# Optimization experiments

Measured on AMD Instinct MI355X. Metric: run time of the kernel, lower is better.

## Reference

```python
import jax, jax.numpy as jnp
from jax import lax
import numpy as np

Vw, Vc, TAGS = 50000, 200, 600
WE, CE, CC, H = 128, 48, 64, 256   # word emb, char emb, char cnn out, encoder hidden
B, T, CL, LMAX = 64, 96, 16, 24    # batch, seq, chars-per-word, lemma max len
HD = H // 2                        # per-direction LSTM hidden
BOS = 3


def _conv1d_same(x, w, b):
    # x: [N, Cin, L], w: [Cout, Cin, K] -> [N, Cout, L]
    y = lax.conv_general_dilated(x, w, (1,), 'SAME', dimension_numbers=('NCH', 'OIH', 'NCH'))
    return y + b[None, :, None]


def _lstm(x, wih, whh, b, reverse):
    # x: [B, T, D]; torch-gate-order LSTM (i, f, g, o); returns [B, T, HD]
    n = x.shape[0]
    def step(carry, xt):
        h, c = carry
        g = xt @ wih.T + h @ whh.T + b
        i, f, gg, o = jnp.split(g, 4, axis=-1)
        c = jax.nn.sigmoid(f) * c + jax.nn.sigmoid(i) * jnp.tanh(gg)
        h = jax.nn.sigmoid(o) * jnp.tanh(c)
        return (h, c), h
    init = (jnp.zeros((n, HD), x.dtype), jnp.zeros((n, HD), x.dtype))
    _, hs = lax.scan(step, init, jnp.swapaxes(x, 0, 1), reverse=reverse)
    return jnp.swapaxes(hs, 0, 1)


def setup_inputs() -> dict:
    key = jax.random.key(0)
    ks = jax.random.split(key, 26)
    g = lambda k, shape: jax.random.normal(k, shape, jnp.float32) * 0.05
    d = {}
    d['word_ids'] = jax.random.randint(ks[0], (B, T), 0, Vw)
    d['char_ids'] = jax.random.randint(ks[1], (B, T, CL), 0, Vc)
    d['word_emb'] = g(ks[2], (Vw, WE)).at[0].set(0.0)          # padding_idx=0
    d['char_emb'] = g(ks[3], (Vc, CE)).at[0].set(0.0)
    d['char_conv_w'] = g(ks[4], (CC, CE, 3))
    d['char_conv_b'] = g(ks[5], (CC,))
    DIN = WE + CC
    d['lstm_fw_wih'] = g(ks[6], (4 * HD, DIN)); d['lstm_fw_whh'] = g(ks[7], (4 * HD, HD)); d['lstm_fw_b'] = g(ks[8], (4 * HD,))
    d['lstm_bw_wih'] = g(ks[9], (4 * HD, DIN)); d['lstm_bw_whh'] = g(ks[10], (4 * HD, HD)); d['lstm_bw_b'] = g(ks[11], (4 * HD,))
    d['tag_w'] = g(ks[12], (TAGS, H)); d['tag_b'] = g(ks[13], (TAGS,))
    d['lemma_emb'] = g(ks[14], (Vc, CE)).at[0].set(0.0)
    d['lemma_init_w'] = g(ks[15], (H, H)); d['lemma_init_b'] = g(ks[16], (H,))
    d['gru_wih'] = g(ks[17], (3 * H, CE)); d['gru_whh'] = g(ks[18], (3 * H, H))
    d['gru_bih'] = g(ks[19], (3 * H,)); d['gru_bhh'] = g(ks[20], (3 * H,))
    d['lemma_proj_w'] = g(ks[21], (Vc, H)); d['lemma_proj_b'] = g(ks[22], (Vc,))
    return d


def reference(word_ids, char_ids, word_emb, char_emb, char_conv_w, char_conv_b,
              lstm_fw_wih, lstm_fw_whh, lstm_fw_b, lstm_bw_wih, lstm_bw_whh, lstm_bw_b,
              tag_w, tag_b, lemma_emb, lemma_init_w, lemma_init_b,
              gru_wih, gru_whh, gru_bih, gru_bhh, lemma_proj_w, lemma_proj_b):
    bsz, tseq = word_ids.shape
    n = bsz * tseq
    # word + char encodings
    wv = word_emb[word_ids]                                   # [B,T,WE]
    ce = char_emb[char_ids].reshape(n, CL, CE)                # [N,CL,CE]
    cv = jax.nn.relu(_conv1d_same(jnp.swapaxes(ce, 1, 2), char_conv_w, char_conv_b)).max(axis=-1)
    enc_in = jnp.concatenate([wv, cv.reshape(bsz, tseq, CC)], axis=-1)
    # BiLSTM encoder
    hf = _lstm(enc_in, lstm_fw_wih, lstm_fw_whh, lstm_fw_b, reverse=False)
    hb = _lstm(enc_in, lstm_bw_wih, lstm_bw_whh, lstm_bw_b, reverse=True)
    enc = jnp.concatenate([hf, hb], axis=-1)                  # [B,T,H]
    tag_logits = enc @ tag_w.T + tag_b
    ef = enc.reshape(n, H)
    h0 = jnp.tanh(ef @ lemma_init_w.T + lemma_init_b)
    prev0 = jnp.full((n,), BOS, dtype=jnp.int32)
    def dec_step(carry, _):
        h, prev = carry
        e = lemma_emb[prev]                                   # [N,CE]
        gi = e @ gru_wih.T + gru_bih
        gh = h @ gru_whh.T + gru_bhh
        ir, iz, inn = jnp.split(gi, 3, axis=-1)
        hr, hz, hn = jnp.split(gh, 3, axis=-1)
        r = jax.nn.sigmoid(ir + hr)
        z = jax.nn.sigmoid(iz + hz)
        nn_ = jnp.tanh(inn + r * hn)
        h = (1.0 - z) * nn_ + z * h
        logits = h @ lemma_proj_w.T + lemma_proj_b            # [N,Vc]
        return (h, jnp.argmax(logits, axis=-1).astype(jnp.int32)), logits
    _, ls = lax.scan(dec_step, (h0, prev0), None, length=LMAX)  # [LMAX,N,Vc]
    lemma_logits = jnp.moveaxis(ls, 0, 1).reshape(bsz, tseq, LMAX, Vc)
    return tag_logits, lemma_logits
```

## Files before the change

kernel.cpp:

```cpp
#include <hip/hip_runtime.h>
#include <hip/hip_bf16.h>
#include <math.h>

typedef float f4 __attribute__((ext_vector_type(4)));
typedef __attribute__((ext_vector_type(8))) short short8;

#define NTAGS 600
#define CEw   48
#define HH    256
#define TSEQ  96
#define CLW   16
#define LMAXD 24
#define NROWS 6144
#define DIN   192
#define VCD   200

__device__ __forceinline__ float sigf(float x){ return 1.0f/(1.0f+expf(-x)); }
__device__ __forceinline__ ushort bhi_u(float v){ __hip_bfloat16 h = __float2bfloat16(v); return *(ushort*)&h; }
__device__ __forceinline__ float ub_f(ushort u){ __hip_bfloat16 h = *(__hip_bfloat16*)&u; return __bfloat162float(h); }

template<int ACT, int HS, int KK>
__global__ __launch_bounds__(256)
void gemm3_k(const ushort* __restrict__ Ahi, const ushort* __restrict__ Alo,
             const ushort* __restrict__ Bhi, const ushort* __restrict__ Blo,
             const float* __restrict__ bias, float* __restrict__ C,
             ushort* __restrict__ Hhi, ushort* __restrict__ Hlo,
             int Nc, int ldC)
{
    __shared__ __align__(16) ushort As[128 * 64];
    __shared__ __align__(16) ushort Bs[128 * 64];
    const int tid = threadIdx.x;
    const int m0 = blockIdx.x * 128;
    const int n0 = blockIdx.y * 128;
    const int w = tid >> 6, l = tid & 63;
    const int wr = (w >> 1) * 64, wc = (w & 1) * 64;
    f4 acc[4][4];
    #pragma unroll
    for (int i = 0; i < 4; ++i)
        #pragma unroll
        for (int j = 0; j < 4; ++j) acc[i][j] = (f4){0.f,0.f,0.f,0.f};

    #pragma unroll
    for (int seg = 0; seg < 3; ++seg) {
        const ushort* Ap = (seg == 1) ? Alo : Ahi;
        const ushort* Bp = (seg == 2) ? Blo : Bhi;
        #pragma unroll
        for (int kt = 0; kt < KK; kt += 64) {
            #pragma unroll
            for (int i = 0; i < 4; ++i) {
                int c = w * 4 + i;
                int row = c * 8 + (l >> 3);
                int col16 = l & 7;
                __builtin_amdgcn_global_load_lds(
                    (const __attribute__((address_space(1))) void*)(Ap + (size_t)(m0 + row) * KK + kt + col16 * 8),
                    (__attribute__((address_space(3))) void*)((char*)As + c * 1024 + l * 16), 16, 0, 0);
                __builtin_amdgcn_global_load_lds(
                    (const __attribute__((address_space(1))) void*)(Bp + (size_t)(n0 + row) * KK + kt + col16 * 8),
                    (__attribute__((address_space(3))) void*)((char*)Bs + c * 1024 + l * 16), 16, 0, 0);
            }
            __syncthreads();
            #pragma unroll
            for (int kk = 0; kk < 64; kk += 32) {
                short8 a[4], b[4];
                #pragma unroll
                for (int mf = 0; mf < 4; ++mf)
                    a[mf] = *(const short8*)(As + (wr + mf * 16 + (l & 15)) * 64 + kk + (l >> 4) * 8);
                #pragma unroll
                for (int nf = 0; nf < 4; ++nf)
                    b[nf] = *(const short8*)(Bs + (wc + nf * 16 + (l & 15)) * 64 + kk + (l >> 4) * 8);
                #pragma unroll
                for (int mf = 0; mf < 4; ++mf)
                    #pragma unroll
                    for (int nf = 0; nf < 4; ++nf)
                        acc[mf][nf] = __builtin_amdgcn_mfma_f32_16x16x32_bf16(a[mf], b[nf], acc[mf][nf], 0, 0, 0);
            }
            __syncthreads();
        }
    }
    #pragma unroll
    for (int nf = 0; nf < 4; ++nf) {
        int n = n0 + wc + nf * 16 + (l & 15);
        if (n >= Nc) continue;
        float bv = bias[n];
        #pragma unroll
        for (int mf = 0; mf < 4; ++mf) {
            int mrow = m0 + wr + mf * 16 + (l >> 4) * 4;
            #pragma unroll
            for (int q2 = 0; q2 < 4; ++q2) {
                float v = acc[mf][nf][q2] + bv;
                if (ACT == 1) v = tanhf(v);
                size_t o = (size_t)(mrow + q2) * ldC + n;
                C[o] = v;
                if (HS) {
                    ushort hi = bhi_u(v);
                    Hhi[o] = hi;
                    Hlo[o] = bhi_u(v - ub_f(hi));
                }
            }
        }
    }
}

__global__ __launch_bounds__(256)
void gemmC_k(const ushort* __restrict__ Ahi, const ushort* __restrict__ Alo,
             const ushort* __restrict__ Bhi, const ushort* __restrict__ Blo,
             const float* __restrict__ bias,
             float* __restrict__ gh, float* __restrict__ lem, int ncol_gh)
{
    __shared__ __align__(16) ushort AsH[64 * 64];
    __shared__ __align__(16) ushort AsL[64 * 64];
    __shared__ __align__(16) ushort BsH[128 * 64];
    __shared__ __align__(16) ushort BsL[128 * 64];
    const int tid = threadIdx.x;
    const int m0 = blockIdx.x * 64;
    const int n0 = blockIdx.y * 128;
    const int w = tid >> 6, l = tid & 63;
    const int wr = (w >> 1) * 32, wc = (w & 1) * 64;
    f4 acc[2][4];
    #pragma unroll
    for (int i = 0; i < 2; ++i)
        #pragma unroll
        for (int j = 0; j < 4; ++j) acc[i][j] = (f4){0.f,0.f,0.f,0.f};

    #pragma unroll
    for (int kt = 0; kt < 256; kt += 64) {
        const int col16 = l & 7;
        #pragma unroll
        for (int i = 0; i < 2; ++i) {
            int c = w * 2 + i;
            int row = c * 8 + (l >> 3);
            size_t ga = (size_t)(m0 + row) * 256 + kt + col16 * 8;
            int loff = c * 1024 + l * 16;
            __builtin_amdgcn_global_load_lds(
                (const __attribute__((address_space(1))) void*)(Ahi + ga),
                (__attribute__((address_space(3))) void*)((char*)AsH + loff), 16, 0, 0);
            __builtin_amdgcn_global_load_lds(
                (const __attribute__((address_space(1))) void*)(Alo + ga),
                (__attribute__((address_space(3))) void*)((char*)AsL + loff), 16, 0, 0);
        }
        #pragma unroll
        for (int i = 0; i < 4; ++i) {
            int c = w * 4 + i;
            int row = c * 8 + (l >> 3);
            size_t gb = (size_t)(n0 + row) * 256 + kt + col16 * 8;
            int loff = c * 1024 + l * 16;
            __builtin_amdgcn_global_load_lds(
                (const __attribute__((address_space(1))) void*)(Bhi + gb),
                (__attribute__((address_space(3))) void*)((char*)BsH + loff), 16, 0, 0);
            __builtin_amdgcn_global_load_lds(
                (const __attribute__((address_space(1))) void*)(Blo + gb),
                (__attribute__((address_space(3))) void*)((char*)BsL + loff), 16, 0, 0);
        }
        __syncthreads();
        #pragma unroll
        for (int kk = 0; kk < 64; kk += 32) {
            short8 ah[2], al[2], bh[4], bl[4];
            #pragma unroll
            for (int mf = 0; mf < 2; ++mf) {
                int off = (wr + mf * 16 + (l & 15)) * 64 + kk + (l >> 4) * 8;
                ah[mf] = *(const short8*)(AsH + off);
                al[mf] = *(const short8*)(AsL + off);
            }
            #pragma unroll
            for (int nf = 0; nf < 4; ++nf) {
                int off = (wc + nf * 16 + (l & 15)) * 64 + kk + (l >> 4) * 8;
                bh[nf] = *(const short8*)(BsH + off);
                bl[nf] = *(const short8*)(BsL + off);
            }
            #pragma unroll
            for (int mf = 0; mf < 2; ++mf)
                #pragma unroll
                for (int nf = 0; nf < 4; ++nf) {
                    acc[mf][nf] = __builtin_amdgcn_mfma_f32_16x16x32_bf16(ah[mf], bh[nf], acc[mf][nf], 0, 0, 0);
                    acc[mf][nf] = __builtin_amdgcn_mfma_f32_16x16x32_bf16(al[mf], bh[nf], acc[mf][nf], 0, 0, 0);
                    acc[mf][nf] = __builtin_amdgcn_mfma_f32_16x16x32_bf16(ah[mf], bl[nf], acc[mf][nf], 0, 0, 0);
                }
        }
        __syncthreads();
    }
    #pragma unroll
    for (int nf = 0; nf < 4; ++nf) {
        int col = n0 + wc + nf * 16 + (l & 15);
        float bv = bias[col];
        #pragma unroll
        for (int mf = 0; mf < 2; ++mf) {
            int mrow = m0 + wr + mf * 16 + (l >> 4) * 4;
            #pragma unroll
            for (int q2 = 0; q2 < 4; ++q2) {
                float v = acc[mf][nf][q2] + bv;
                int m = mrow + q2;
                if (col < ncol_gh) {
                    gh[(size_t)m * 768 + col] = v;
                } else {
                    int c2 = col - ncol_gh;
                    if (c2 < VCD && lem)
                        lem[(size_t)m * (LMAXD * VCD) + c2] = v;
                }
            }
        }
    }
}

__global__ __launch_bounds__(256)
void argupd_k(const float* __restrict__ gh, const float* __restrict__ git,
              const float* __restrict__ lem,
              ushort* __restrict__ hhi, ushort* __restrict__ hlo)
{
    const int bid = blockIdx.x;
    const int x = bid & 7, r = bid >> 3;
    const int i = r >> 6, jrow = r & 63;
    const int n = ((x + (i << 3)) << 6) + jrow;
    const int tid = threadIdx.x;
    __shared__ float sv[4];
    __shared__ int   si[4];
    __shared__ int   sprev;
    if (lem) {
        float v = (tid < VCD) ? lem[(size_t)n * (LMAXD * VCD) + tid] : -3.4e38f;
        int bi = tid;
        #pragma unroll
        for (int d = 1; d < 64; d <<= 1) {
            float ov = __shfl_xor(v, d);
            int   oi = __shfl_xor(bi, d);
            if (ov > v || (ov == v && oi < bi)) { v = ov; bi = oi; }
        }
        if ((tid & 63) == 0) { sv[tid >> 6] = v; si[tid >> 6] = bi; }
        __syncthreads();
        if (tid == 0) {
            float b = sv[0]; int bi2 = si[0];
            #pragma unroll
            for (int t2 = 1; t2 < 4; ++t2)
                if (sv[t2] > b || (sv[t2] == b && si[t2] < bi2)) { b = sv[t2]; bi2 = si[t2]; }
            sprev = bi2;
        }
    } else if (tid == 0) sprev = 3;
    __syncthreads();
    const int prev = sprev;
    const int j = tid;
    const float* g  = gh + (size_t)n * 768;
    const float* gi = git + (size_t)prev * 768;
    float rg = sigf(gi[j] + g[j]);
    float z  = sigf(gi[256 + j] + g[256 + j]);
    float nn = tanhf(gi[512 + j] + rg * g[512 + j]);
    size_t o = (size_t)n * HH + j;
    float hold = ub_f(hhi[o]) + ub_f(hlo[o]);
    float hv = (1.0f - z) * nn + z * hold;
    ushort hi = bhi_u(hv);
    hhi[o] = hi;
    hlo[o] = bhi_u(hv - ub_f(hi));
}

__global__ __launch_bounds__(256)
void conv_k(const ushort* __restrict__ cehi, const ushort* __restrict__ celo,
            const ushort* __restrict__ wre, const float* __restrict__ conv_b,
            float* __restrict__ enc_in)
{
    __shared__ __align__(16) ushort Bs[2 * 64 * 192];
    const int tid = threadIdx.x;
    for (int i = tid; i < 2 * 64 * 192 / 8; i += 256)
        ((uint4*)Bs)[i] = ((const uint4*)wre)[i];
    __syncthreads();
    const int w = tid >> 6, l = tid & 63;
    const int p = l & 15, g = l >> 4;
    const int base = (blockIdx.x * 4 + w) * 8;
    for (int wi = 0; wi < 8; ++wi) {
        int n = base + wi;
        short8 ahi[6], alo[6];
        #pragma unroll
        for (int kt = 0; kt < 6; ++kt) {
            int t = kt >> 1;
            int e0 = (kt & 1) * 32 + g * 8;
            int rl = p + t - 1;
            bool val = (rl >= 0 && rl < 16);
            size_t off = (size_t)(n * 16 + rl) * 64 + e0;
            short8 z = (short8){0,0,0,0,0,0,0,0};
            ahi[kt] = val ? *(const short8*)(cehi + off) : z;
            alo[kt] = val ? *(const short8*)(celo + off) : z;
        }
        f4 acc[4];
        #pragma unroll
        for (int nf = 0; nf < 4; ++nf) acc[nf] = (f4){0.f,0.f,0.f,0.f};
        #pragma unroll
        for (int kt = 0; kt < 6; ++kt) {
            #pragma unroll
            for (int nf = 0; nf < 4; ++nf) {
                int boff = (nf * 16 + (l & 15)) * 192 + kt * 32 + g * 8;
                short8 bh = *(const short8*)(Bs + boff);
                short8 bl = *(const short8*)(Bs + 12288 + boff);
                acc[nf] = __builtin_amdgcn_mfma_f32_16x16x32_bf16(ahi[kt], bh, acc[nf], 0, 0, 0);
                acc[nf] = __builtin_amdgcn_mfma_f32_16x16x32_bf16(alo[kt], bh, acc[nf], 0, 0, 0);
                acc[nf] = __builtin_amdgcn_mfma_f32_16x16x32_bf16(ahi[kt], bl, acc[nf], 0, 0, 0);
            }
        }
        #pragma unroll
        for (int nf = 0; nf < 4; ++nf) {
            float m = fmaxf(fmaxf(acc[nf][0], acc[nf][1]), fmaxf(acc[nf][2], acc[nf][3]));
            m = fmaxf(m, __shfl_xor(m, 16));
            m = fmaxf(m, __shfl_xor(m, 32));
            if (l < 16) {
                int c = nf * 16 + l;
                enc_in[(size_t)n * DIN + 128 + c] = fmaxf(0.0f, m + conv_b[c]);
            }
        }
    }
}

__global__ void repack192_k(const float* __restrict__ w, __hip_bfloat16* __restrict__ wre)
{
    int idx = blockIdx.x * 256 + threadIdx.x;
    if (idx >= 64 * 192) return;
    int kk = idx % 192, c = idx / 192;
    int t = kk >> 6, e = kk & 63;
    float v = (e < 48) ? w[(c * 48 + e) * 3 + t] : 0.0f;
    __hip_bfloat16 hi = __float2bfloat16(v);
    wre[idx] = hi;
    wre[64 * 192 + idx] = __float2bfloat16(v - __bfloat162float(hi));
}

__global__ void ce64_k(const int* __restrict__ char_ids, const float* __restrict__ char_emb,
                       __hip_bfloat16* __restrict__ hi, __hip_bfloat16* __restrict__ lo)
{
    size_t idx = (size_t)blockIdx.x * 256 + threadIdx.x;
    if (idx >= (size_t)NROWS * CLW * 64) return;
    int e = idx & 63;
    size_t r = idx >> 6;
    float v = (e < 48) ? char_emb[(size_t)char_ids[r] * CEw + e] : 0.0f;
    __hip_bfloat16 h = __float2bfloat16(v);
    hi[idx] = h;
    lo[idx] = __float2bfloat16(v - __bfloat162float(h));
}

__global__ void wv_k(const int* __restrict__ wid, const float* __restrict__ wemb,
                     float* __restrict__ enc_in)
{
    size_t idx = (size_t)blockIdx.x * 256 + threadIdx.x;
    if (idx >= (size_t)NROWS * 128) return;
    int e = idx & 127; size_t n = idx >> 7;
    enc_in[n * DIN + e] = wemb[(size_t)wid[n] * 128 + e];
}

__global__ void eisplit_k(const float* __restrict__ x, __hip_bfloat16* __restrict__ hi,
                          __hip_bfloat16* __restrict__ lo)
{
    size_t idx = (size_t)blockIdx.x * 256 + threadIdx.x;
    if (idx >= (size_t)NROWS * DIN) return;
    float v = x[idx];
    __hip_bfloat16 h = __float2bfloat16(v);
    hi[idx] = h;
    lo[idx] = __float2bfloat16(v - __bfloat162float(h));
}

__global__ void wsplit_k(const float* __restrict__ W, __hip_bfloat16* __restrict__ out,
                         int rows, int rowsPad, int K)
{
    int idx = blockIdx.x * 256 + threadIdx.x;
    if (idx >= rowsPad * K) return;
    int r = idx / K, k = idx - r * K;
    float v = (r < rows) ? W[(size_t)r * K + k] : 0.0f;
    __hip_bfloat16 hi = __float2bfloat16(v);
    out[idx] = hi;
    out[rowsPad * K + idx] = __float2bfloat16(v - __bfloat162float(hi));
}

__global__ void cmbsplit_k(const float* __restrict__ whh, const float* __restrict__ proj,
                           const float* __restrict__ bhh, const float* __restrict__ pb,
                           __hip_bfloat16* __restrict__ out, float* __restrict__ cbias)
{
    int idx = blockIdx.x * 256 + threadIdx.x;
    if (idx >= 1024 * 256) return;
    int r = idx >> 8, k = idx & 255;
    float v = (r < 768) ? whh[(size_t)r * 256 + k] : ((r < 968) ? proj[(size_t)(r - 768) * 256 + k] : 0.0f);
    __hip_bfloat16 hi = __float2bfloat16(v);
    out[idx] = hi;
    out[1024 * 256 + idx] = __float2bfloat16(v - __bfloat162float(hi));
    if (idx < 1024)
        cbias[idx] = (idx < 768) ? bhh[idx] : ((idx < 968) ? pb[idx - 768] : 0.0f);
}

__global__ void whht_k(const float* __restrict__ fw, const float* __restrict__ bw,
                       float* __restrict__ out)
{
    int idx = blockIdx.x * 256 + threadIdx.x;
    if (idx >= 131072) return;
    int q = idx & 3, j = (idx >> 2) & 127, k = (idx >> 9) & 127, d = idx >> 16;
    const float* w = d ? bw : fw;
    out[idx] = w[(size_t)(q * 128 + j) * 128 + k];
}

__global__ void gitab_k(const float* __restrict__ lemb, const float* __restrict__ wih,
                        const float* __restrict__ bih, float* __restrict__ git)
{
    int idx = blockIdx.x * 256 + threadIdx.x;
    if (idx >= VCD * 768) return;
    int g = idx % 768, v = idx / 768;
    float s = bih[g];
    #pragma unroll
    for (int k = 0; k < CEw; ++k) s = fmaf(lemb[v * CEw + k], wih[(size_t)g * CEw + k], s);
    git[idx] = s;
}

__global__ __launch_bounds__(1024, 4)
void lstm_k(const float* __restrict__ gi2, const float* __restrict__ whht,
            __hip_bfloat16* __restrict__ enc_hi, __hip_bfloat16* __restrict__ enc_lo)
{
    const int dir = blockIdx.x >> 6, b = blockIdx.x & 63;
    const int tid = threadIdx.x;
    const int j = tid & 127, q = tid >> 7;
    const float* gi = gi2 + (size_t)dir * NROWS * 512;
    const f4* wt = (const f4*)(whht + (size_t)dir * 65536);
    f4 wreg[16];
    #pragma unroll
    for (int kk = 0; kk < 16; ++kk) wreg[kk] = wt[(q * 16 + kk) * 128 + j];
    __shared__ float hbuf[128];
    __shared__ f4 part[8][128];
    float c = 0.0f;
    if (tid < 128) hbuf[tid] = 0.0f;
    float nai = 0.f, naf = 0.f, nag = 0.f, nao = 0.f;
    if (q == 0) {
        int t0 = dir ? (TSEQ - 1) : 0;
        const float* gr = gi + ((size_t)b * TSEQ + t0) * 512;
        nai = gr[j]; naf = gr[128 + j]; nag = gr[256 + j]; nao = gr[384 + j];
    }
    __syncthreads();
    for (int s = 0; s < TSEQ; ++s) {
        int t = dir ? (TSEQ - 1 - s) : s;
        size_t n = (size_t)b * TSEQ + t;
        float ai = nai, af = naf, ag = nag, ao = nao;
        const f4* hb = (const f4*)(hbuf + q * 16);
        f4 hh[4] = {hb[0], hb[1], hb[2], hb[3]};
        f4 p = (f4){0.f,0.f,0.f,0.f};
        #pragma unroll
        for (int kk = 0; kk < 16; ++kk) {
            float hv = hh[kk >> 2][kk & 3];
            p.x = fmaf(wreg[kk].x, hv, p.x);
            p.y = fmaf(wreg[kk].y, hv, p.y);
            p.z = fmaf(wreg[kk].z, hv, p.z);
            p.w = fmaf(wreg[kk].w, hv, p.w);
        }
        part[q][j] = p;
        __syncthreads();
        if (q == 0) {
            f4 sum = part[0][j];
            #pragma unroll
            for (int qq = 1; qq < 8; ++qq) {
                f4 pp = part[qq][j];
                sum.x += pp.x; sum.y += pp.y; sum.z += pp.z; sum.w += pp.w;
            }
            ai += sum.x; af += sum.y; ag += sum.z; ao += sum.w;
            c = sigf(af) * c + sigf(ai) * tanhf(ag);
            float h = sigf(ao) * tanhf(c);
            hbuf[j] = h;
            size_t o = n * HH + dir * 128 + j;
            __hip_bfloat16 hi = __float2bfloat16(h);
            enc_hi[o] = hi;
            enc_lo[o] = __float2bfloat16(h - __bfloat162float(hi));
            if (s + 1 < TSEQ) {
                int t2 = dir ? (TSEQ - 2 - s) : (s + 1);
                const float* gr2 = gi + ((size_t)b * TSEQ + t2) * 512;
                nai = gr2[j]; naf = gr2[128 + j]; nag = gr2[256 + j]; nao = gr2[384 + j];
            }
        }
        __syncthreads();
    }
}

extern "C" void kernel_launch(void* const* d_in, const int* in_sizes, int n_in,
                              void* d_out, int out_size, void* d_ws, size_t ws_size,
                              hipStream_t stream)
{
    const int*   word_ids = (const int*)d_in[0];
    const int*   char_ids = (const int*)d_in[1];
    const float* word_emb = (const float*)d_in[2];
    const float* char_emb = (const float*)d_in[3];
    const float* conv_w   = (const float*)d_in[4];
    const float* conv_b   = (const float*)d_in[5];
    const float* fw_wih   = (const float*)d_in[6];
    const float* fw_whh   = (const float*)d_in[7];
    const float* fw_b     = (const float*)d_in[8];
    const float* bw_wih   = (const float*)d_in[9];
    const float* bw_whh   = (const float*)d_in[10];
    const float* bw_b     = (const float*)d_in[11];
    const float* tag_w    = (const float*)d_in[12];
    const float* tag_b    = (const float*)d_in[13];
    const float* lemma_emb= (const float*)d_in[14];
    const float* init_w   = (const float*)d_in[15];
    const float* init_b   = (const float*)d_in[16];
    const float* gru_wih  = (const float*)d_in[17];
    const float* gru_whh  = (const float*)d_in[18];
    const float* gru_bih  = (const float*)d_in[19];
    const float* gru_bhh  = (const float*)d_in[20];
    const float* proj_w   = (const float*)d_in[21];
    const float* proj_b   = (const float*)d_in[22];

    char* ws = (char*)d_ws;
    float* enc_in = (float*)(ws);
    __hip_bfloat16* ei_hi = (__hip_bfloat16*)(ws + 4718592);
    __hip_bfloat16* ei_lo = (__hip_bfloat16*)(ws + 7077888);
    __hip_bfloat16* enc_hi = (__hip_bfloat16*)(ws);
    __hip_bfloat16* enc_lo = (__hip_bfloat16*)(ws + 3145728);
    char* R1 = ws + 9437184;
    __hip_bfloat16* ce_hi = (__hip_bfloat16*)R1;
    __hip_bfloat16* ce_lo = (__hip_bfloat16*)(R1 + 12582912);
    float* gi2 = (float*)R1;
    float* gh  = (float*)R1;
    __hip_bfloat16* cmb_ext = (__hip_bfloat16*)(R1 + 18874368);
    float* cmb_bias = (float*)(R1 + 18874368 + 1048576);
    float* hdec = (float*)(ws + 34603008);
    __hip_bfloat16* h_hi = (__hip_bfloat16*)(ws + 40894464);
    __hip_bfloat16* h_lo = (__hip_bfloat16*)(ws + 44040192);
    float* git  = (float*)(ws + 47185920);
    float* whht = (float*)(ws + 47800320);
    __hip_bfloat16* wre_ext  = (__hip_bfloat16*)(ws + 48349184);
    __hip_bfloat16* wfw_ext  = (__hip_bfloat16*)(ws + 48398336);
    __hip_bfloat16* wbw_ext  = (__hip_bfloat16*)(ws + 48791552);
    __hip_bfloat16* tag_ext  = (__hip_bfloat16*)(ws + 49184768);
    __hip_bfloat16* init_ext = (__hip_bfloat16*)(ws + 49840128);

    float* out_tag = (float*)d_out;
    float* out_lem = out_tag + (size_t)NROWS * NTAGS;

    repack192_k<<<48, 256, 0, stream>>>(conv_w, wre_ext);
    ce64_k<<<24576, 256, 0, stream>>>(char_ids, char_emb, ce_hi, ce_lo);
    wv_k<<<3072, 256, 0, stream>>>(word_ids, word_emb, enc_in);
    conv_k<<<192, 256, 0, stream>>>((const ushort*)ce_hi, (const ushort*)ce_lo,
                                    (const ushort*)wre_ext, conv_b, enc_in);
    eisplit_k<<<4608, 256, 0, stream>>>(enc_in, ei_hi, ei_lo);
    wsplit_k<<<384, 256, 0, stream>>>(fw_wih, wfw_ext, 512, 512, 192);
    wsplit_k<<<384, 256, 0, stream>>>(bw_wih, wbw_ext, 512, 512, 192);

    gemm3_k<0,0,192><<<dim3(48,4), 256, 0, stream>>>((const ushort*)ei_hi, (const ushort*)ei_lo,
        (const ushort*)wfw_ext, (const ushort*)(wfw_ext + 512*192), fw_b, gi2,
        nullptr, nullptr, 512, 512);
    gemm3_k<0,0,192><<<dim3(48,4), 256, 0, stream>>>((const ushort*)ei_hi, (const ushort*)ei_lo,
        (const ushort*)wbw_ext, (const ushort*)(wbw_ext + 512*192), bw_b, gi2 + (size_t)NROWS*512,
        nullptr, nullptr, 512, 512);
    whht_k<<<512, 256, 0, stream>>>(fw_whh, bw_whh, whht);
    lstm_k<<<128, 1024, 0, stream>>>(gi2, whht, enc_hi, enc_lo);

    cmbsplit_k<<<1024, 256, 0, stream>>>(gru_whh, proj_w, gru_bhh, proj_b, cmb_ext, cmb_bias);
    wsplit_k<<<640, 256, 0, stream>>>(tag_w, tag_ext, 600, 640, 256);
    wsplit_k<<<256, 256, 0, stream>>>(init_w, init_ext, 256, 256, 256);
    gitab_k<<<600, 256, 0, stream>>>(lemma_emb, gru_wih, gru_bih, git);
    gemm3_k<0,0,256><<<dim3(48,5), 256, 0, stream>>>((const ushort*)enc_hi, (const ushort*)enc_lo,
        (const ushort*)tag_ext, (const ushort*)(tag_ext + 640*256), tag_b, out_tag,
        nullptr, nullptr, NTAGS, NTAGS);
    gemm3_k<1,1,256><<<dim3(48,2), 256, 0, stream>>>((const ushort*)enc_hi, (const ushort*)enc_lo,
        (const ushort*)init_ext, (const ushort*)(init_ext + 256*256), init_b, hdec,
        (ushort*)h_hi, (ushort*)h_lo, 256, 256);

    const ushort* cmb_hi = (const ushort*)cmb_ext;
    const ushort* cmb_lo = cmb_hi + 1024 * 256;
    for (int s = 0; s < LMAXD; ++s) {
        float* lem = (s > 0) ? (out_lem + (size_t)(s - 1) * VCD) : nullptr;
        gemmC_k<<<dim3(96,8), 256, 0, stream>>>((const ushort*)h_hi, (const ushort*)h_lo,
            cmb_hi, cmb_lo, cmb_bias, gh, lem, 768);
        argupd_k<<<NROWS, 256, 0, stream>>>(gh, git, lem, (ushort*)h_hi, (ushort*)h_lo);
    }
    gemmC_k<<<dim3(96,2), 256, 0, stream>>>((const ushort*)h_hi, (const ushort*)h_lo,
        cmb_hi + 768 * 256, cmb_lo + 768 * 256, cmb_bias + 768,
        nullptr, out_lem + (size_t)(LMAXD - 1) * VCD, 0);
}
```

Baseline: 916.0 us.

## Fuse GRU update and argmax into decoder GEMM kernel with ping-pong buffers

```diff
diff --git a/kernel.cpp b/kernel.cpp
--- a/kernel.cpp
+++ b/kernel.cpp
@@ -95,6 +95,168 @@
                     ushort hi = bhi_u(v);
                     Hhi[o] = hi;
                     Hlo[o] = bhi_u(v - ub_f(hi));
+                }
+            }
+        }
+    }
+}
+
+__global__ __launch_bounds__(256)
+void dec_k(float* __restrict__ ghW, const float* __restrict__ ghR,
+           const ushort* __restrict__ hRhi, const ushort* __restrict__ hRlo,
+           ushort* __restrict__ hWhi, ushort* __restrict__ hWlo,
+           const float* __restrict__ git,
+           const ushort* __restrict__ Bhi, const ushort* __restrict__ Blo,
+           const float* __restrict__ bias, float* __restrict__ out_lem,
+           int t, int n0base)
+{
+    __shared__ __align__(16) char smem[49152];
+    ushort* Bsm = (ushort*)(smem + 32768);
+    __shared__ int sprev[32];
+    const int tid = threadIdx.x;
+    const int m0 = blockIdx.x * 32;
+    const int n0 = n0base + blockIdx.y * 128;
+
+    if (t >= 2) {
+        int r = tid >> 3, c = tid & 7;
+        const float* L = out_lem + ((size_t)(m0 + r) * LMAXD + (t - 2)) * VCD;
+        float best = -3.4e38f; int bi = 0;
+        for (int i = c; i < VCD; i += 8) {
+            float v = L[i];
+            if (v > best) { best = v; bi = i; }
+        }
+        #pragma unroll
+        for (int d = 1; d < 8; d <<= 1) {
+            float ov = __shfl_xor(best, d);
+            int   oi = __shfl_xor(bi, d);
+            if (ov > best || (ov == best && oi < bi)) { best = ov; bi = oi; }
+        }
+        if (c == 0) sprev[r] = bi;
+        __syncthreads();
+    } else if (t == 1) {
+        if (tid < 32) sprev[tid] = 3;
+        __syncthreads();
+    }
+
+    if (t == 0) {
+        #pragma unroll 4
+        for (int i = 0; i < 32; ++i) {
+            size_t o = (size_t)(m0 + i) * 256 + tid;
+            int so = i * 512 + ((2 * tid) ^ ((i & 7) << 4));
+            *(ushort*)(smem + so) = hRhi[o];
+            *(ushort*)(smem + 16384 + so) = hRlo[o];
+        }
+    } else {
+        #pragma unroll 2
+        for (int i = 0; i < 32; ++i) {
+            int row = m0 + i;
+            const float* g  = ghR + (size_t)row * 768;
+            const float* gi = git + (size_t)sprev[i] * 768;
+            int j = tid;
+            float rg = sigf(gi[j] + g[j]);
+            float z  = sigf(gi[256 + j] + g[256 + j]);
+            float nn = tanhf(gi[512 + j] + rg * g[512 + j]);
+            size_t o = (size_t)row * 256 + j;
+            float hold = ub_f(hRhi[o]) + ub_f(hRlo[o]);
+            float hv = (1.0f - z) * nn + z * hold;
+            ushort hi = bhi_u(hv);
+            ushort lo = bhi_u(hv - ub_f(hi));
+            hWhi[o] = hi;
+            hWlo[o] = lo;
+            int so = i * 512 + ((2 * j) ^ ((i & 7) << 4));
+            *(ushort*)(smem + so) = hi;
+            *(ushort*)(smem + 16384 + so) = lo;
+        }
+    }
+    __syncthreads();
+
+    const int w = tid >> 6, l = tid & 63;
+    const int wc = w * 32;
+    const int lr = l & 15;
+    const int lk = (l >> 4) * 8;
+    f4 acc[2][2];
+    #pragma unroll
+    for (int i = 0; i < 2; ++i)
+        #pragma unroll
+        for (int j = 0; j < 2; ++j) acc[i][j] = (f4){0.f,0.f,0.f,0.f};
+
+    #pragma unroll
+    for (int kt = 0; kt < 256; kt += 64) {
+        short8 ah[2][2], al[2][2];
+        #pragma unroll
+        for (int mf = 0; mf < 2; ++mf)
+            #pragma unroll
+            for (int kx = 0; kx < 2; ++kx) {
+                int row = mf * 16 + lr;
+                int j0 = kt + kx * 32 + lk;
+                int so = row * 512 + ((2 * j0) ^ ((row & 7) << 4));
+                ah[mf][kx] = *(const short8*)(smem + so);
+                al[mf][kx] = *(const short8*)(smem + 16384 + so);
+            }
+        #pragma unroll
+        for (int i = 0; i < 4; ++i) {
+            int c = w * 4 + i;
+            int brow = c * 8 + (l >> 3);
+            __builtin_amdgcn_global_load_lds(
+                (const __attribute__((address_space(1))) void*)(Bhi + (size_t)(n0 + brow) * 256 + kt + (l & 7) * 8),
+                (__attribute__((address_space(3))) void*)(smem + 32768 + c * 1024 + l * 16), 16, 0, 0);
+        }
+        __syncthreads();
+        #pragma unroll
+        for (int kx = 0; kx < 2; ++kx) {
+            short8 bh[2];
+            #pragma unroll
+            for (int nf = 0; nf < 2; ++nf)
+                bh[nf] = *(const short8*)(Bsm + (wc + nf * 16 + lr) * 64 + kx * 32 + lk);
+            #pragma unroll
+            for (int mf = 0; mf < 2; ++mf)
+                #pragma unroll
+                for (int nf = 0; nf < 2; ++nf) {
+                    acc[mf][nf] = __builtin_amdgcn_mfma_f32_16x16x32_bf16(ah[mf][kx], bh[nf], acc[mf][nf], 0, 0, 0);
+                    acc[mf][nf] = __builtin_amdgcn_mfma_f32_16x16x32_bf16(al[mf][kx], bh[nf], acc[mf][nf], 0, 0, 0);
+                }
+        }
+        __syncthreads();
+        #pragma unroll
+        for (int i = 0; i < 4; ++i) {
+            int c = w * 4 + i;
+            int brow = c * 8 + (l >> 3);
+            __builtin_amdgcn_global_load_lds(
+                (const __attribute__((address_space(1))) void*)(Blo + (size_t)(n0 + brow) * 256 + kt + (l & 7) * 8),
+                (__attribute__((address_space(3))) void*)(smem + 32768 + c * 1024 + l * 16), 16, 0, 0);
+        }
+        __syncthreads();
+        #pragma unroll
+        for (int kx = 0; kx < 2; ++kx) {
+            short8 bl[2];
+            #pragma unroll
+            for (int nf = 0; nf < 2; ++nf)
+                bl[nf] = *(const short8*)(Bsm + (wc + nf * 16 + lr) * 64 + kx * 32 + lk);
+            #pragma unroll
+            for (int mf = 0; mf < 2; ++mf)
+                #pragma unroll
+                for (int nf = 0; nf < 2; ++nf)
+                    acc[mf][nf] = __builtin_amdgcn_mfma_f32_16x16x32_bf16(ah[mf][kx], bl[nf], acc[mf][nf], 0, 0, 0);
+        }
+        __syncthreads();
+    }
+    #pragma unroll
+    for (int nf = 0; nf < 2; ++nf) {
+        int col = n0 + wc + nf * 16 + lr;
+        float bv = bias[col];
+        #pragma unroll
+        for (int mf = 0; mf < 2; ++mf) {
+            int mrow = m0 + mf * 16 + (l >> 4) * 4;
+            #pragma unroll
+            for (int q2 = 0; q2 < 4; ++q2) {
+                float v = acc[mf][nf][q2] + bv;
+                int m = mrow + q2;
+                if (col < 768) {
+                    ghW[(size_t)m * 768 + col] = v;
+                } else {
+                    int c2 = col - 768;
+                    if (c2 < VCD && t > 0)
+                        out_lem[((size_t)m * LMAXD + (t - 1)) * VCD + c2] = v;
                 }
             }
         }
@@ -492,31 +654,68 @@
     const float* proj_b   = (const float*)d_in[22];
 
     char* ws = (char*)d_ws;
-    float* enc_in = (float*)(ws);
-    __hip_bfloat16* ei_hi = (__hip_bfloat16*)(ws + 4718592);
-    __hip_bfloat16* ei_lo = (__hip_bfloat16*)(ws + 7077888);
-    __hip_bfloat16* enc_hi = (__hip_bfloat16*)(ws);
-    __hip_bfloat16* enc_lo = (__hip_bfloat16*)(ws + 3145728);
-    char* R1 = ws + 9437184;
-    __hip_bfloat16* ce_hi = (__hip_bfloat16*)R1;
-    __hip_bfloat16* ce_lo = (__hip_bfloat16*)(R1 + 12582912);
-    float* gi2 = (float*)R1;
-    float* gh  = (float*)R1;
-    __hip_bfloat16* cmb_ext = (__hip_bfloat16*)(R1 + 18874368);
-    float* cmb_bias = (float*)(R1 + 18874368 + 1048576);
-    float* hdec = (float*)(ws + 34603008);
-    __hip_bfloat16* h_hi = (__hip_bfloat16*)(ws + 40894464);
-    __hip_bfloat16* h_lo = (__hip_bfloat16*)(ws + 44040192);
-    float* git  = (float*)(ws + 47185920);
-    float* whht = (float*)(ws + 47800320);
-    __hip_bfloat16* wre_ext  = (__hip_bfloat16*)(ws + 48349184);
-    __hip_bfloat16* wfw_ext  = (__hip_bfloat16*)(ws + 48398336);
-    __hip_bfloat16* wbw_ext  = (__hip_bfloat16*)(ws + 48791552);
-    __hip_bfloat16* tag_ext  = (__hip_bfloat16*)(ws + 49184768);
-    __hip_bfloat16* init_ext = (__hip_bfloat16*)(ws + 49840128);
-
     float* out_tag = (float*)d_out;
     float* out_lem = out_tag + (size_t)NROWS * NTAGS;
+
+    const bool fused = (ws_size >= 51998720ull);
+
+    float *enc_in, *gi2, *whht, *git, *cmb_bias, *hdec_scratch;
+    __hip_bfloat16 *ce_hi, *ce_lo, *ei_hi, *ei_lo, *enc_hi, *enc_lo;
+    __hip_bfloat16 *wre_ext, *wfw_ext, *wbw_ext, *tag_ext, *init_ext, *cmb_ext;
+    ushort *b0_hi, *b0_lo, *b1_hi, *b1_lo;
+    float *ghA, *ghB;
+
+    if (fused) {
+        ce_hi = (__hip_bfloat16*)(ws + 0);
+        ce_lo = (__hip_bfloat16*)(ws + 12582912);
+        enc_in = (float*)(ws + 25165824);
+        wre_ext = (__hip_bfloat16*)(ws + 29884416);
+        wfw_ext = (__hip_bfloat16*)(ws + 29933568);
+        wbw_ext = (__hip_bfloat16*)(ws + 30326784);
+        ei_hi = (__hip_bfloat16*)(ws + 30720000);
+        ei_lo = (__hip_bfloat16*)(ws + 33079296);
+        whht = (float*)(ws + 35438592);
+        tag_ext = (__hip_bfloat16*)(ws + 35962880);
+        init_ext = (__hip_bfloat16*)(ws + 36618240);
+        gi2 = (float*)(ws + 0);
+        enc_hi = (__hip_bfloat16*)(ws + 25165824);
+        enc_lo = (__hip_bfloat16*)(ws + 28311552);
+        hdec_scratch = (float*)(ws + 0);
+        ghA = (float*)(ws + 0);
+        ghB = (float*)(ws + 18874368);
+        b0_hi = (ushort*)(ws + 37748736);
+        b0_lo = (ushort*)(ws + 40894464);
+        b1_hi = (ushort*)(ws + 44040192);
+        b1_lo = (ushort*)(ws + 47185920);
+        git = (float*)(ws + 50331648);
+        cmb_ext = (__hip_bfloat16*)(ws + 50946048);
+        cmb_bias = (float*)(ws + 51994624);
+    } else {
+        enc_in = (float*)(ws);
+        ei_hi = (__hip_bfloat16*)(ws + 4718592);
+        ei_lo = (__hip_bfloat16*)(ws + 7077888);
+        enc_hi = (__hip_bfloat16*)(ws);
+        enc_lo = (__hip_bfloat16*)(ws + 3145728);
+        char* R1 = ws + 9437184;
+        ce_hi = (__hip_bfloat16*)R1;
+        ce_lo = (__hip_bfloat16*)(R1 + 12582912);
+        gi2 = (float*)R1;
+        ghA = (float*)R1;
+        ghB = ghA;
+        cmb_ext = (__hip_bfloat16*)(R1 + 18874368);
+        cmb_bias = (float*)(R1 + 18874368 + 1048576);
+        hdec_scratch = (float*)(ws + 34603008);
+        b0_hi = (ushort*)(ws + 40894464);
+        b0_lo = (ushort*)(ws + 44040192);
+        b1_hi = b0_hi; b1_lo = b0_lo;
+        git = (float*)(ws + 47185920);
+        whht = (float*)(ws + 47800320);
+        wre_ext = (__hip_bfloat16*)(ws + 48349184);
+        wfw_ext = (__hip_bfloat16*)(ws + 48398336);
+        wbw_ext = (__hip_bfloat16*)(ws + 48791552);
+        tag_ext = (__hip_bfloat16*)(ws + 49184768);
+        init_ext = (__hip_bfloat16*)(ws + 49840128);
+    }
 
     repack192_k<<<48, 256, 0, stream>>>(conv_w, wre_ext);
     ce64_k<<<24576, 256, 0, stream>>>(char_ids, char_emb, ce_hi, ce_lo);
@@ -544,18 +743,37 @@
         (const ushort*)tag_ext, (const ushort*)(tag_ext + 640*256), tag_b, out_tag,
         nullptr, nullptr, NTAGS, NTAGS);
     gemm3_k<1,1,256><<<dim3(48,2), 256, 0, stream>>>((const ushort*)enc_hi, (const ushort*)enc_lo,
-        (const ushort*)init_ext, (const ushort*)(init_ext + 256*256), init_b, hdec,
-        (ushort*)h_hi, (ushort*)h_lo, 256, 256);
+        (const ushort*)init_ext, (const ushort*)(init_ext + 256*256), init_b, hdec_scratch,
+        b0_hi, b0_lo, 256, 256);
 
     const ushort* cmb_hi = (const ushort*)cmb_ext;
     const ushort* cmb_lo = cmb_hi + 1024 * 256;
-    for (int s = 0; s < LMAXD; ++s) {
-        float* lem = (s > 0) ? (out_lem + (size_t)(s - 1) * VCD) : nullptr;
-        gemmC_k<<<dim3(96,8), 256, 0, stream>>>((const ushort*)h_hi, (const ushort*)h_lo,
-            cmb_hi, cmb_lo, cmb_bias, gh, lem, 768);
-        argupd_k<<<NROWS, 256, 0, stream>>>(gh, git, lem, (ushort*)h_hi, (ushort*)h_lo);
-    }
-    gemmC_k<<<dim3(96,2), 256, 0, stream>>>((const ushort*)h_hi, (const ushort*)h_lo,
-        cmb_hi + 768 * 256, cmb_lo + 768 * 256, cmb_bias + 768,
-        nullptr, out_lem + (size_t)(LMAXD - 1) * VCD, 0);
-}
+
+    if (fused) {
+        float* ghbuf[2] = {ghA, ghB};
+        ushort* hb_hi[2] = {b0_hi, b1_hi};
+        ushort* hb_lo[2] = {b0_lo, b1_lo};
+        for (int t = 0; t <= 24; ++t) {
+            float* ghW = ghbuf[t & 1];
+            const float* ghR = ghbuf[(t ^ 1) & 1];
+            int rp = (t == 0) ? 0 : ((t - 1) & 1);
+            int wp = t & 1;
+            dim3 grid = (t == 0) ? dim3(192, 6) : ((t == 24) ? dim3(192, 2) : dim3(192, 8));
+            int n0base = (t == 24) ? 768 : 0;
+            dec_k<<<grid, 256, 0, stream>>>(ghW, ghR,
+                hb_hi[rp], hb_lo[rp], hb_hi[wp], hb_lo[wp],
+                git, cmb_hi, cmb_lo, cmb_bias, out_lem, t, n0base);
+        }
+    } else {
+        float* gh = ghA;
+        for (int s = 0; s < LMAXD; ++s) {
+            float* lem = (s > 0) ? (out_lem + (size_t)(s - 1) * VCD) : nullptr;
+            gemmC_k<<<dim3(96,8), 256, 0, stream>>>((const ushort*)b0_hi, (const ushort*)b0_lo,
+                cmb_hi, cmb_lo, cmb_bias, gh, lem, 768);
+            argupd_k<<<NROWS, 256, 0, stream>>>(gh, git, lem, b0_hi, b0_lo);
+        }
+        gemmC_k<<<dim3(96,2), 256, 0, stream>>>((const ushort*)b0_hi, (const ushort*)b0_lo,
+            cmb_hi + 768 * 256, cmb_lo + 768 * 256, cmb_bias + 768,
+            nullptr, out_lem + (size_t)(LMAXD - 1) * VCD, 0);
+    }
+}
```

After: 1.723 ms. +88.1%, slower.

## Fuse char embedding gather into conv kernel and spread LSTM gate activations

Applied to the files above, without the earlier changes.

```diff
diff --git a/kernel.cpp b/kernel.cpp
--- a/kernel.cpp
+++ b/kernel.cpp
@@ -250,7 +250,7 @@
 }
 
 __global__ __launch_bounds__(256)
-void conv_k(const ushort* __restrict__ cehi, const ushort* __restrict__ celo,
+void conv_k(const int* __restrict__ char_ids, const float* __restrict__ char_emb,
             const ushort* __restrict__ wre, const float* __restrict__ conv_b,
             float* __restrict__ enc_in)
 {
@@ -270,11 +270,26 @@
             int t = kt >> 1;
             int e0 = (kt & 1) * 32 + g * 8;
             int rl = p + t - 1;
-            bool val = (rl >= 0 && rl < 16);
-            size_t off = (size_t)(n * 16 + rl) * 64 + e0;
-            short8 z = (short8){0,0,0,0,0,0,0,0};
-            ahi[kt] = val ? *(const short8*)(cehi + off) : z;
-            alo[kt] = val ? *(const short8*)(celo + off) : z;
+            bool val = (rl >= 0 && rl < 16) && (e0 < 48);
+            short8 zh = (short8){0,0,0,0,0,0,0,0};
+            short8 zl = zh;
+            if (val) {
+                int cid = char_ids[n * 16 + rl];
+                const float* src = char_emb + (size_t)cid * CEw + e0;
+                f4 v0 = *(const f4*)(src);
+                f4 v1 = *(const f4*)(src + 4);
+                #pragma unroll
+                for (int i2 = 0; i2 < 4; ++i2) {
+                    ushort h0 = bhi_u(v0[i2]);
+                    ushort h1 = bhi_u(v1[i2]);
+                    zh[i2] = (short)h0;
+                    zh[i2 + 4] = (short)h1;
+                    zl[i2] = (short)bhi_u(v0[i2] - ub_f(h0));
+                    zl[i2 + 4] = (short)bhi_u(v1[i2] - ub_f(h1));
+                }
+            }
+            ahi[kt] = zh;
+            alo[kt] = zl;
         }
         f4 acc[4];
         #pragma unroll
@@ -314,19 +329,6 @@
     __hip_bfloat16 hi = __float2bfloat16(v);
     wre[idx] = hi;
     wre[64 * 192 + idx] = __float2bfloat16(v - __bfloat162float(hi));
-}
-
-__global__ void ce64_k(const int* __restrict__ char_ids, const float* __restrict__ char_emb,
-                       __hip_bfloat16* __restrict__ hi, __hip_bfloat16* __restrict__ lo)
-{
-    size_t idx = (size_t)blockIdx.x * 256 + threadIdx.x;
-    if (idx >= (size_t)NROWS * CLW * 64) return;
-    int e = idx & 63;
-    size_t r = idx >> 6;
-    float v = (e < 48) ? char_emb[(size_t)char_ids[r] * CEw + e] : 0.0f;
-    __hip_bfloat16 h = __float2bfloat16(v);
-    hi[idx] = h;
-    lo[idx] = __float2bfloat16(v - __bfloat162float(h));
 }
 
 __global__ void wv_k(const int* __restrict__ wid, const float* __restrict__ wemb,
@@ -412,19 +414,18 @@
     for (int kk = 0; kk < 16; ++kk) wreg[kk] = wt[(q * 16 + kk) * 128 + j];
     __shared__ float hbuf[128];
     __shared__ f4 part[8][128];
+    __shared__ float act[4][128];
     float c = 0.0f;
     if (tid < 128) hbuf[tid] = 0.0f;
-    float nai = 0.f, naf = 0.f, nag = 0.f, nao = 0.f;
-    if (q == 0) {
+    float gnext = 0.0f;
+    if (q < 4) {
         int t0 = dir ? (TSEQ - 1) : 0;
-        const float* gr = gi + ((size_t)b * TSEQ + t0) * 512;
-        nai = gr[j]; naf = gr[128 + j]; nag = gr[256 + j]; nao = gr[384 + j];
+        gnext = gi[((size_t)b * TSEQ + t0) * 512 + q * 128 + j];
     }
     __syncthreads();
     for (int s = 0; s < TSEQ; ++s) {
         int t = dir ? (TSEQ - 1 - s) : s;
         size_t n = (size_t)b * TSEQ + t;
-        float ai = nai, af = naf, ag = nag, ao = nao;
         const f4* hb = (const f4*)(hbuf + q * 16);
         f4 hh[4] = {hb[0], hb[1], hb[2], hb[3]};
         f4 p = (f4){0.f,0.f,0.f,0.f};
@@ -438,26 +439,35 @@
         }
         part[q][j] = p;
         __syncthreads();
-        if (q == 0) {
-            f4 sum = part[0][j];
+        if (q < 4) {
+            f4 sv = part[0][j];
             #pragma unroll
             for (int qq = 1; qq < 8; ++qq) {
                 f4 pp = part[qq][j];
-                sum.x += pp.x; sum.y += pp.y; sum.z += pp.z; sum.w += pp.w;
-            }
-            ai += sum.x; af += sum.y; ag += sum.z; ao += sum.w;
-            c = sigf(af) * c + sigf(ai) * tanhf(ag);
-            float h = sigf(ao) * tanhf(c);
+                sv.x += pp.x; sv.y += pp.y; sv.z += pp.z; sv.w += pp.w;
+            }
+            float sum;
+            if (q == 0)      sum = sv.x;
+            else if (q == 1) sum = sv.y;
+            else if (q == 2) sum = sv.z;
+            else             sum = sv.w;
+            float pre = gnext + sum;
+            act[q][j] = (q == 2) ? tanhf(pre) : sigf(pre);
+            if (s + 1 < TSEQ) {
+                int t2 = dir ? (TSEQ - 2 - s) : (s + 1);
+                gnext = gi[((size_t)b * TSEQ + t2) * 512 + q * 128 + j];
+            }
+        }
+        __syncthreads();
+        if (q == 0) {
+            float ai_ = act[0][j], af_ = act[1][j], ag_ = act[2][j], ao_ = act[3][j];
+            c = af_ * c + ai_ * ag_;
+            float h = ao_ * tanhf(c);
             hbuf[j] = h;
             size_t o = n * HH + dir * 128 + j;
             __hip_bfloat16 hi = __float2bfloat16(h);
             enc_hi[o] = hi;
             enc_lo[o] = __float2bfloat16(h - __bfloat162float(hi));
-            if (s + 1 < TSEQ) {
-                int t2 = dir ? (TSEQ - 2 - s) : (s + 1);
-                const float* gr2 = gi + ((size_t)b * TSEQ + t2) * 512;
-                nai = gr2[j]; naf = gr2[128 + j]; nag = gr2[256 + j]; nao = gr2[384 + j];
-            }
         }
         __syncthreads();
     }
@@ -498,8 +508,6 @@
     __hip_bfloat16* enc_hi = (__hip_bfloat16*)(ws);
     __hip_bfloat16* enc_lo = (__hip_bfloat16*)(ws + 3145728);
     char* R1 = ws + 9437184;
-    __hip_bfloat16* ce_hi = (__hip_bfloat16*)R1;
-    __hip_bfloat16* ce_lo = (__hip_bfloat16*)(R1 + 12582912);
     float* gi2 = (float*)R1;
     float* gh  = (float*)R1;
     __hip_bfloat16* cmb_ext = (__hip_bfloat16*)(R1 + 18874368);
@@ -519,9 +527,8 @@
     float* out_lem = out_tag + (size_t)NROWS * NTAGS;
 
     repack192_k<<<48, 256, 0, stream>>>(conv_w, wre_ext);
-    ce64_k<<<24576, 256, 0, stream>>>(char_ids, char_emb, ce_hi, ce_lo);
     wv_k<<<3072, 256, 0, stream>>>(word_ids, word_emb, enc_in);
-    conv_k<<<192, 256, 0, stream>>>((const ushort*)ce_hi, (const ushort*)ce_lo,
+    conv_k<<<192, 256, 0, stream>>>(char_ids, char_emb,
                                     (const ushort*)wre_ext, conv_b, enc_in);
     eisplit_k<<<4608, 256, 0, stream>>>(enc_in, ei_hi, ei_lo);
     wsplit_k<<<384, 256, 0, stream>>>(fw_wih, wfw_ext, 512, 512, 192);
```

Result: faster. 897.3 us (-2.1%).
